# Optimization experiments

Measured on AMD Instinct MI355X. Metric: run time of the kernel, lower is better.

Reference implementation:

```python
import jax, jax.numpy as jnp
import numpy as np

N_NODES = 100000
NEG_SLOPE = 0.2


def _gat_conv(x, edge_index, W, att_src, att_dst, bias):
    """Single-head PyG-style GATConv with self-loops.
    x: [N, F_in], edge_index: [2, E] (row 0 = src j, row 1 = dst i).
    """
    N = x.shape[0]
    h = x @ W  # [N, F_out]
    # add self-loops
    loop = jnp.arange(N, dtype=edge_index.dtype)
    src = jnp.concatenate([edge_index[0], loop])
    dst = jnp.concatenate([edge_index[1], loop])
    # per-node attention terms, gathered per edge
    a_s = h @ att_src  # [N]
    a_d = h @ att_dst  # [N]
    e = jax.nn.leaky_relu(a_s[src] + a_d[dst], NEG_SLOPE)  # [E+N]
    # segment softmax over incoming edges of each destination
    m = jax.ops.segment_max(e, dst, num_segments=N)  # [N]
    m = jnp.where(jnp.isfinite(m), m, 0.0)
    p = jnp.exp(e - m[dst])
    denom = jax.ops.segment_sum(p, dst, num_segments=N)  # [N], >0 due to self-loops
    alpha = p / denom[dst]  # [E+N]
    # scatter-aggregate weighted source features
    out = jax.ops.segment_sum(h[src] * alpha[:, None], dst, num_segments=N)
    return out + bias


def setup_inputs() -> dict:
    key = jax.random.key(0)
    ks = jax.random.split(key, 12)
    F_in, H, C = 128, 64, 40
    x = jax.random.normal(ks[0], (N_NODES, F_in), dtype=jnp.float32)
    edge_index = jax.random.randint(ks[1], (2, 1600000), 0, N_NODES, dtype=jnp.int64)
    s1 = 1.0 / np.sqrt(F_in)
    s2 = 1.0 / np.sqrt(H)
    return {
        "x": x,
        "edge_index": edge_index,
        "W1": jax.random.uniform(ks[2], (F_in, H), jnp.float32, -s1, s1),
        "att_src1": jax.random.uniform(ks[3], (H,), jnp.float32, -s2, s2),
        "att_dst1": jax.random.uniform(ks[4], (H,), jnp.float32, -s2, s2),
        "b1": jnp.zeros((H,), jnp.float32),
        "W2": jax.random.uniform(ks[5], (H, C), jnp.float32, -s2, s2),
        "att_src2": jax.random.uniform(ks[6], (C,), jnp.float32, -1.0 / np.sqrt(C), 1.0 / np.sqrt(C)),
        "att_dst2": jax.random.uniform(ks[7], (C,), jnp.float32, -1.0 / np.sqrt(C), 1.0 / np.sqrt(C)),
        "b2": jnp.zeros((C,), jnp.float32),
    }


def reference(x, edge_index, W1, att_src1, att_dst1, b1, W2, att_src2, att_dst2, b2):
    h = _gat_conv(x, edge_index, W1, att_src1, att_dst1, b1)
    h = jax.nn.relu(h)
    # dropout is identity in eval mode
    out = _gat_conv(h, edge_index, W2, att_src2, att_dst2, b2)
    return out
```

## Files before the change

kernel.cpp:

```cpp
#include <hip/hip_runtime.h>
#include <math.h>


#define NEG_SLOPE 0.2f
#define BIN_SHIFT 10
#define BIN_NODES 1024
#define MAXBINS   128
#define CAPB      17408
#define K1_CHUNK  4096
#define MAXDEG    128
#define AGG_STRIDE 132

typedef _Float16 h4_t __attribute__((ext_vector_type(4)));
typedef _Float16 h8_t __attribute__((ext_vector_type(8)));
typedef float    f16x_t __attribute__((ext_vector_type(16)));

__device__ __forceinline__ float lrelu(float v) {
    return v > 0.f ? v : NEG_SLOPE * v;
}

__global__ __launch_bounds__(256) void prep_kernel(
    const float* __restrict__ W1, const float* __restrict__ W2,
    _Float16* __restrict__ w1t, _Float16* __restrict__ w2t)
{
    const int tid = threadIdx.x;
    for (int i = tid; i < 8192; i += 256) {
        int n = i >> 7, k = i & 127;
        w1t[i] = (_Float16)W1[k * 64 + n];
    }
    for (int i = tid; i < 4096; i += 256) {
        int n = i >> 6, k = i & 63;
        w2t[i] = (n < 40) ? (_Float16)W2[k * 40 + n] : (_Float16)0.f;
    }
}

__global__ __launch_bounds__(256) void bin_kernel(
    const int* __restrict__ src, const int* __restrict__ dst, int E, int nbins,
    int* __restrict__ bin_cursor, int* __restrict__ binned)
{
    __shared__ int hist[MAXBINS];
    __shared__ int base[MAXBINS];
    __shared__ int lcur[MAXBINS];
    const int tid = threadIdx.x;
    const int e0 = blockIdx.x * K1_CHUNK;

    if (tid < nbins) hist[tid] = 0;
    __syncthreads();

    for (int k = tid; k < K1_CHUNK; k += 256) {
        int e = e0 + k;
        if (e < E) atomicAdd(&hist[dst[e] >> BIN_SHIFT], 1);
    }
    __syncthreads();

    if (tid < nbins) {
        int c = hist[tid];
        base[tid] = (c > 0) ? atomicAdd(&bin_cursor[tid], c) : 0;
        lcur[tid] = 0;
    }
    __syncthreads();

    for (int k = tid; k < K1_CHUNK; k += 256) {
        int e = e0 + k;
        if (e < E) {
            int d = dst[e];
            int s = src[e];
            int b = d >> BIN_SHIFT;
            int o = atomicAdd(&lcur[b], 1);
            int pos = base[b] + o;
            if (pos < CAPB)
                binned[b * CAPB + pos] = (s << BIN_SHIFT) | (d & (BIN_NODES - 1));
        }
    }
}

__global__ __launch_bounds__(128) void scan_kernel(
    const int* __restrict__ bin_cursor, int* __restrict__ bin_base, int nbins)
{
    __shared__ int a[MAXBINS];
    const int tid = threadIdx.x;
    int v = (tid < nbins) ? min(bin_cursor[tid], CAPB) : 0;
    a[tid] = v;
    __syncthreads();
#pragma unroll
    for (int ofs = 1; ofs < 128; ofs <<= 1) {
        int t = (tid >= ofs) ? a[tid - ofs] : 0;
        __syncthreads();
        a[tid] += t;
        __syncthreads();
    }
    if (tid < nbins) bin_base[tid] = a[tid] - v;
}

__global__ __launch_bounds__(1024) void fine_kernel(
    const int* __restrict__ bin_cursor, const int* __restrict__ bin_base,
    const int* __restrict__ binned,
    int* __restrict__ csr, int* __restrict__ rowptr, int N, int nbins)
{
    __shared__ int a[BIN_NODES];
    __shared__ int cur[BIN_NODES];
    const int b = blockIdx.x;
    const int tid = threadIdx.x;

    const int cnt = min(bin_cursor[b], CAPB);
    const int binbase = bin_base[b];
    const int nn = min(BIN_NODES, N - b * BIN_NODES);
    const int* __restrict__ brec = binned + (long)b * CAPB;

    a[tid] = 0;
    __syncthreads();

    for (int k = tid; k < cnt; k += 1024) {
        atomicAdd(&a[brec[k] & (BIN_NODES - 1)], 1);
    }
    __syncthreads();

    int v = a[tid];
#pragma unroll
    for (int ofs = 1; ofs < BIN_NODES; ofs <<= 1) {
        int t = (tid >= ofs) ? a[tid - ofs] : 0;
        __syncthreads();
        a[tid] += t;
        __syncthreads();
    }
    const int excl = a[tid] - v;

    if (tid < nn) rowptr[b * BIN_NODES + tid] = binbase + excl;
    cur[tid] = binbase + excl;
    if (b == nbins - 1 && tid == 0) rowptr[N] = binbase + cnt;
    __syncthreads();

    for (int k = tid; k < cnt; k += 1024) {
        int rec = brec[k];
        int pos = atomicAdd(&cur[rec & (BIN_NODES - 1)], 1);
        csr[pos] = rec >> BIN_SHIFT;
    }
}

#define XS1 136
__global__ __launch_bounds__(256) void gemm1_kernel(
    const float* __restrict__ x, const _Float16* __restrict__ w1t,
    const float* __restrict__ att_s, const float* __restrict__ att_d,
    _Float16* __restrict__ h, float* __restrict__ as_, float* __restrict__ ad_,
    int N)
{
    __shared__ __align__(16) _Float16 Xs[64 * XS1];
    __shared__ __align__(16) _Float16 Wt[64 * XS1];
    __shared__ float psrow[64], pdrow[64];
    const int tid = threadIdx.x;
    const int lane = tid & 63;
    const int w = tid >> 6;
    const int rh = w >> 1, ch = w & 1;
    const long rowbase = (long)blockIdx.x * 64;

    {
        const int4* src = (const int4*)w1t;
#pragma unroll
        for (int i = 0; i < 4; ++i) {
            int f = tid + i * 256;
            int n = f >> 4, c = f & 15;
            *(int4*)&Wt[n * XS1 + c * 8] = src[f];
        }
    }
    {
        const float4* X4 = (const float4*)x;
        const long gmax = (long)N * 32;
#pragma unroll
        for (int i = 0; i < 8; ++i) {
            int f = tid + i * 256;
            int row = f >> 5, c4 = f & 31;
            long gi = (rowbase + row) * 32 + c4;
            float4 v = (gi < gmax) ? X4[gi] : make_float4(0.f, 0.f, 0.f, 0.f);
            h4_t hv;
            hv.x = (_Float16)v.x; hv.y = (_Float16)v.y;
            hv.z = (_Float16)v.z; hv.w = (_Float16)v.w;
            *(h4_t*)&Xs[row * XS1 + c4 * 4] = hv;
        }
    }
    if (tid < 64) { psrow[tid] = 0.f; pdrow[tid] = 0.f; }
    __syncthreads();

    const int m = lane & 31, khalf = lane >> 5;
    const _Float16* ax = &Xs[(rh * 32 + m) * XS1 + khalf * 8];
    const _Float16* bx = &Wt[(ch * 32 + m) * XS1 + khalf * 8];

    f16x_t acc = {};
#pragma unroll
    for (int kc = 0; kc < 8; ++kc) {
        h8_t a = *(const h8_t*)(ax + kc * 16);
        h8_t b = *(const h8_t*)(bx + kc * 16);
        acc = __builtin_amdgcn_mfma_f32_32x32x16_f16(a, b, acc, 0, 0, 0);
    }

    const int col = ch * 32 + m;
    const float asc = att_s[col], adc = att_d[col];
#pragma unroll
    for (int r = 0; r < 16; ++r) {
        int rowl = (r & 3) + 8 * (r >> 2) + 4 * khalf;
        long grow = rowbase + rh * 32 + rowl;
        float v = acc[r];
        if (grow < N) h[grow * 64 + col] = (_Float16)v;
        float ps = v * asc, pd = v * adc;
#pragma unroll
        for (int off = 1; off < 32; off <<= 1) {
            ps += __shfl_xor(ps, off);
            pd += __shfl_xor(pd, off);
        }
        if (m == 0) {
            atomicAdd(&psrow[rh * 32 + rowl], ps);
            atomicAdd(&pdrow[rh * 32 + rowl], pd);
        }
    }
    __syncthreads();
    if (tid < 64) {
        long grow = rowbase + tid;
        if (grow < N) { as_[grow] = psrow[tid]; ad_[grow] = pdrow[tid]; }
    }
}

#define XS2 72
__global__ __launch_bounds__(256) void gemm2_kernel(
    const _Float16* __restrict__ hin, const _Float16* __restrict__ w2t,
    const float* __restrict__ att_s, const float* __restrict__ att_d,
    _Float16* __restrict__ h2, float* __restrict__ as_, float* __restrict__ ad_,
    int N)
{
    __shared__ __align__(16) _Float16 Xs[64 * XS2];
    __shared__ __align__(16) _Float16 Wt[64 * XS2];
    __shared__ float psrow[64], pdrow[64];
    const int tid = threadIdx.x;
    const int lane = tid & 63;
    const int w = tid >> 6;
    const int rh = w >> 1, ch = w & 1;
    const long rowbase = (long)blockIdx.x * 64;

    {
        const int4* src = (const int4*)w2t;
#pragma unroll
        for (int i = 0; i < 2; ++i) {
            int f = tid + i * 256;
            int n = f >> 3, c = f & 7;
            *(int4*)&Wt[n * XS2 + c * 8] = src[f];
        }
    }
    {
        const h8_t* X8 = (const h8_t*)hin;
        const long gmax = (long)N * 8;
#pragma unroll
        for (int i = 0; i < 2; ++i) {
            int f = tid + i * 256;
            int row = f >> 3, c = f & 7;
            long gi = (rowbase + row) * 8 + c;
            h8_t v = {};
            if (gi < gmax) v = X8[gi];
#pragma unroll
            for (int j = 0; j < 8; ++j) v[j] = (v[j] > (_Float16)0.f) ? v[j] : (_Float16)0.f;
            *(h8_t*)&Xs[row * XS2 + c * 8] = v;
        }
    }
    if (tid < 64) { psrow[tid] = 0.f; pdrow[tid] = 0.f; }
    __syncthreads();

    const int m = lane & 31, khalf = lane >> 5;
    const _Float16* ax = &Xs[(rh * 32 + m) * XS2 + khalf * 8];
    const _Float16* bx = &Wt[(ch * 32 + m) * XS2 + khalf * 8];

    f16x_t acc = {};
#pragma unroll
    for (int kc = 0; kc < 4; ++kc) {
        h8_t a = *(const h8_t*)(ax + kc * 16);
        h8_t b = *(const h8_t*)(bx + kc * 16);
        acc = __builtin_amdgcn_mfma_f32_32x32x16_f16(a, b, acc, 0, 0, 0);
    }

    const int col = ch * 32 + m;
    const bool cval = (col < 40);
    const float asc = cval ? att_s[col] : 0.f;
    const float adc = cval ? att_d[col] : 0.f;
#pragma unroll
    for (int r = 0; r < 16; ++r) {
        int rowl = (r & 3) + 8 * (r >> 2) + 4 * khalf;
        long grow = rowbase + rh * 32 + rowl;
        float v = acc[r];
        if (cval && grow < N) h2[grow * 40 + col] = (_Float16)v;
        float ps = v * asc, pd = v * adc;
#pragma unroll
        for (int off = 1; off < 32; off <<= 1) {
            ps += __shfl_xor(ps, off);
            pd += __shfl_xor(pd, off);
        }
        if (m == 0) {
            atomicAdd(&psrow[rh * 32 + rowl], ps);
            atomicAdd(&pdrow[rh * 32 + rowl], pd);
        }
    }
    __syncthreads();
    if (tid < 64) {
        long grow = rowbase + tid;
        if (grow < N) { as_[grow] = psrow[tid]; ad_[grow] = pdrow[tid]; }
    }
}

template<int F, typename OT>
__global__ __launch_bounds__(256) void aggregate_kernel(
    const _Float16* __restrict__ h, const float* __restrict__ as_,
    const float* __restrict__ ad_, const int* __restrict__ rowptr,
    const int* __restrict__ csr, const float* __restrict__ bias,
    OT* __restrict__ out, int N)
{
    __shared__ int   Ss[16 * AGG_STRIDE];
    __shared__ float Ps[16 * AGG_STRIDE];
    const int tid = threadIdx.x;
    const int dl  = tid >> 4;
    const int sub = tid & 15;
    const int i = blockIdx.x * 16 + dl;
    const bool alive = (i < N);

    int r0 = 0, deg = 0;
    if (alive) {
        r0 = rowptr[i];
        deg = rowptr[i + 1] - r0;
        if (deg > MAXDEG) deg = MAXDEG;
    }
    const float adi    = alive ? ad_[i] : 0.f;
    const float e_self = alive ? lrelu(as_[i] + adi) : 0.f;

    int*   __restrict__ sp = &Ss[dl * AGG_STRIDE];
    float* __restrict__ pp = &Ps[dl * AGG_STRIDE];

    float psum = 0.f;
    for (int c = sub; c < deg; c += 16) {
        int s = csr[r0 + c];
        float p = __expf(lrelu(as_[s] + adi));
        sp[c] = s;
        pp[c] = p;
        psum += p;
    }
#pragma unroll
    for (int off = 1; off < 16; off <<= 1) psum += __shfl_xor(psum, off);
    const float p_self = __expf(e_self);
    const float inv = 1.f / (psum + p_self);

    const bool act = (sub * 4 < F);
    const int  col = act ? sub * 4 : 0;
    float4 acc = make_float4(0.f, 0.f, 0.f, 0.f);

    int k = 0;
    for (; k + 4 <= deg; k += 4) {
        int   sA = sp[k],     sB = sp[k + 1], sC = sp[k + 2], sD = sp[k + 3];
        float pA = pp[k],     pB = pp[k + 1], pC = pp[k + 2], pD = pp[k + 3];
        if (act) {
            h4_t hA = *(const h4_t*)&h[(long)sA * F + col];
            h4_t hB = *(const h4_t*)&h[(long)sB * F + col];
            h4_t hC = *(const h4_t*)&h[(long)sC * F + col];
            h4_t hD = *(const h4_t*)&h[(long)sD * F + col];
            acc.x += (float)hA.x * pA + (float)hB.x * pB + (float)hC.x * pC + (float)hD.x * pD;
            acc.y += (float)hA.y * pA + (float)hB.y * pB + (float)hC.y * pC + (float)hD.y * pD;
            acc.z += (float)hA.z * pA + (float)hB.z * pB + (float)hC.z * pC + (float)hD.z * pD;
            acc.w += (float)hA.w * pA + (float)hB.w * pB + (float)hC.w * pC + (float)hD.w * pD;
        }
    }
    for (; k < deg; ++k) {
        int   s = sp[k];
        float p = pp[k];
        if (act) {
            h4_t hv = *(const h4_t*)&h[(long)s * F + col];
            acc.x += (float)hv.x * p; acc.y += (float)hv.y * p;
            acc.z += (float)hv.z * p; acc.w += (float)hv.w * p;
        }
    }

    if (alive && act) {
        h4_t hv = *(const h4_t*)&h[(long)i * F + col];
        float4 bv = *(const float4*)&bias[col];
        float ox = (acc.x + (float)hv.x * p_self) * inv + bv.x;
        float oy = (acc.y + (float)hv.y * p_self) * inv + bv.y;
        float oz = (acc.z + (float)hv.z * p_self) * inv + bv.z;
        float ow = (acc.w + (float)hv.w * p_self) * inv + bv.w;
        if constexpr (sizeof(OT) == 4) {
            float4 o = make_float4(ox, oy, oz, ow);
            *(float4*)&out[(long)i * F + col] = o;
        } else {
            h4_t o;
            o.x = (_Float16)ox; o.y = (_Float16)oy;
            o.z = (_Float16)oz; o.w = (_Float16)ow;
            *(h4_t*)&out[(long)i * F + col] = o;
        }
    }
}

extern "C" void kernel_launch(void* const* d_in, const int* in_sizes, int n_in,
                              void* d_out, int out_size, void* d_ws, size_t ws_size,
                              hipStream_t stream) {
    const float* x    = (const float*)d_in[0];
    const int*   ei   = (const int*)d_in[1];
    const float* W1   = (const float*)d_in[2];
    const float* at_s1= (const float*)d_in[3];
    const float* at_d1= (const float*)d_in[4];
    const float* b1   = (const float*)d_in[5];
    const float* W2   = (const float*)d_in[6];
    const float* at_s2= (const float*)d_in[7];
    const float* at_d2= (const float*)d_in[8];
    const float* b2   = (const float*)d_in[9];
    float* out = (float*)d_out;

    const int N = in_sizes[0] / 128;
    const int E = in_sizes[1] / 2;
    const int nbins = (N + BIN_NODES - 1) >> BIN_SHIFT;

    char* p = (char*)d_ws;
    auto carve = [&](size_t bytes) -> void* {
        void* r = (void*)p;
        p += (bytes + 255) & ~(size_t)255;
        return r;
    };
    int*       bin_cursor = (int*)      carve((size_t)MAXBINS * 4);
    int*       bin_base   = (int*)      carve((size_t)MAXBINS * 4);
    int*       binned     = (int*)      carve((size_t)nbins * CAPB * 4);
    int*       csr        = (int*)      carve((size_t)E * 4);
    int*       rowptr     = (int*)      carve((size_t)(N + 1) * 4);
    _Float16*  w1t        = (_Float16*) carve((size_t)8192 * 2);
    _Float16*  w2t        = (_Float16*) carve((size_t)4096 * 2);
    _Float16*  h1         = (_Float16*) carve((size_t)N * 64 * 2);
    _Float16*  agg1h      = (_Float16*) carve((size_t)N * 64 * 2);
    _Float16*  h2         = (_Float16*) carve((size_t)N * 40 * 2);
    float*     asn        = (float*)    carve((size_t)N * 4);
    float*     adn        = (float*)    carve((size_t)N * 4);

    hipMemsetAsync(bin_cursor, 0, (size_t)MAXBINS * 4, stream);

    prep_kernel<<<1, 256, 0, stream>>>(W1, W2, w1t, w2t);
    bin_kernel<<<(E + K1_CHUNK - 1) / K1_CHUNK, 256, 0, stream>>>(
        ei, ei + E, E, nbins, bin_cursor, binned);
    scan_kernel<<<1, 128, 0, stream>>>(bin_cursor, bin_base, nbins);
    fine_kernel<<<nbins, 1024, 0, stream>>>(bin_cursor, bin_base, binned, csr, rowptr, N, nbins);

    gemm1_kernel<<<(N + 63) / 64, 256, 0, stream>>>(x, w1t, at_s1, at_d1, h1, asn, adn, N);
    aggregate_kernel<64, _Float16><<<(N + 15) / 16, 256, 0, stream>>>(
        h1, asn, adn, rowptr, csr, b1, agg1h, N);

    gemm2_kernel<<<(N + 63) / 64, 256, 0, stream>>>(agg1h, w2t, at_s2, at_d2, h2, asn, adn, N);
    aggregate_kernel<40, float><<<(N + 15) / 16, 256, 0, stream>>>(
        h2, asn, adn, rowptr, csr, b2, out, N);
}
```

Baseline: 271.6 us.

## Fuse gemm1 with edge binning and fold attention vectors into weights

Attention projections are precomputed as W·att vectors. Layer 1 computes a_s/a_d directly from x with a small dot product. Layer 2 appends them as two extra MFMA output columns in the padded weight tile, which removes the per-row shuffle reductions and LDS atomics. The gemm1 and edge-binning kernels are merged into a single launch with a block-range split so both run concurrently, and the binning path now preloads its edges into registers. The cost is a larger shared-memory footprint for the merged kernel, plus extra fp16 rounding of the folded attention vectors in layer 2 and of x in layer 1.

Result: faster. 241.4 us (-11.1%).

```diff
diff --git a/kernel.cpp b/kernel.cpp
--- a/kernel.cpp
+++ b/kernel.cpp
@@ -10,6 +10,7 @@
 #define K1_CHUNK  4096
 #define MAXDEG    128
 #define AGG_STRIDE 132
+#define XS1 136
 
 typedef _Float16 h4_t __attribute__((ext_vector_type(4)));
 typedef _Float16 h8_t __attribute__((ext_vector_type(8)));
@@ -21,55 +22,175 @@
 
 __global__ __launch_bounds__(256) void prep_kernel(
     const float* __restrict__ W1, const float* __restrict__ W2,
-    _Float16* __restrict__ w1t, _Float16* __restrict__ w2t)
-{
-    const int tid = threadIdx.x;
-    for (int i = tid; i < 8192; i += 256) {
-        int n = i >> 7, k = i & 127;
-        w1t[i] = (_Float16)W1[k * 64 + n];
-    }
-    for (int i = tid; i < 4096; i += 256) {
-        int n = i >> 6, k = i & 63;
-        w2t[i] = (n < 40) ? (_Float16)W2[k * 40 + n] : (_Float16)0.f;
-    }
-}
-
-__global__ __launch_bounds__(256) void bin_kernel(
+    const float* __restrict__ as1, const float* __restrict__ ad1,
+    const float* __restrict__ as2, const float* __restrict__ ad2,
+    _Float16* __restrict__ w1t, _Float16* __restrict__ w2t,
+    float* __restrict__ u1, float* __restrict__ v1)
+{
+    const int tid = threadIdx.x;
+    if (blockIdx.x == 0) {
+        for (int i = tid; i < 8192; i += 256) {
+            int n = i >> 7, k = i & 127;
+            w1t[i] = (_Float16)W1[k * 64 + n];
+        }
+        if (tid < 128) {
+            float su = 0.f, sv = 0.f;
+            for (int n = 0; n < 64; ++n) {
+                float w = W1[tid * 64 + n];
+                su += w * as1[n];
+                sv += w * ad1[n];
+            }
+            u1[tid] = su; v1[tid] = sv;
+        }
+    } else {
+        __shared__ float u2l[64], v2l[64];
+        if (tid < 64) {
+            float su = 0.f, sv = 0.f;
+            for (int n = 0; n < 40; ++n) {
+                float w = W2[tid * 40 + n];
+                su += w * as2[n];
+                sv += w * ad2[n];
+            }
+            u2l[tid] = su; v2l[tid] = sv;
+        }
+        __syncthreads();
+        for (int i = tid; i < 4096; i += 256) {
+            int n = i >> 6, k = i & 63;
+            _Float16 o = (_Float16)0.f;
+            if (n < 40)       o = (_Float16)W2[k * 40 + n];
+            else if (n == 40) o = (_Float16)u2l[k];
+            else if (n == 41) o = (_Float16)v2l[k];
+            w2t[i] = o;
+        }
+    }
+}
+
+__global__ __launch_bounds__(256) void gemm1_bin_kernel(
+    const float* __restrict__ x, const _Float16* __restrict__ w1t,
+    const float* __restrict__ u1, const float* __restrict__ v1,
+    _Float16* __restrict__ h, float* __restrict__ as_, float* __restrict__ ad_,
+    int N, int gb,
     const int* __restrict__ src, const int* __restrict__ dst, int E, int nbins,
     int* __restrict__ bin_cursor, int* __restrict__ binned)
 {
-    __shared__ int hist[MAXBINS];
-    __shared__ int base[MAXBINS];
-    __shared__ int lcur[MAXBINS];
-    const int tid = threadIdx.x;
-    const int e0 = blockIdx.x * K1_CHUNK;
-
-    if (tid < nbins) hist[tid] = 0;
-    __syncthreads();
-
-    for (int k = tid; k < K1_CHUNK; k += 256) {
-        int e = e0 + k;
-        if (e < E) atomicAdd(&hist[dst[e] >> BIN_SHIFT], 1);
-    }
-    __syncthreads();
-
-    if (tid < nbins) {
-        int c = hist[tid];
-        base[tid] = (c > 0) ? atomicAdd(&bin_cursor[tid], c) : 0;
-        lcur[tid] = 0;
-    }
-    __syncthreads();
-
-    for (int k = tid; k < K1_CHUNK; k += 256) {
-        int e = e0 + k;
-        if (e < E) {
-            int d = dst[e];
-            int s = src[e];
-            int b = d >> BIN_SHIFT;
-            int o = atomicAdd(&lcur[b], 1);
-            int pos = base[b] + o;
-            if (pos < CAPB)
-                binned[b * CAPB + pos] = (s << BIN_SHIFT) | (d & (BIN_NODES - 1));
+    __shared__ __align__(16) char smem[35840];
+    const int tid = threadIdx.x;
+
+    if (blockIdx.x < gb) {
+        _Float16* Xs = (_Float16*)smem;
+        _Float16* Wt = (_Float16*)(smem + 17408);
+        float*    Us = (float*)(smem + 34816);
+        float*    Vs = (float*)(smem + 35328);
+        const int lane = tid & 63;
+        const int w = tid >> 6;
+        const int rh = w >> 1, ch = w & 1;
+        const long rowbase = (long)blockIdx.x * 64;
+
+        {
+            const int4* s4 = (const int4*)w1t;
+#pragma unroll
+            for (int i = 0; i < 4; ++i) {
+                int f = tid + i * 256;
+                int n = f >> 4, c = f & 15;
+                *(int4*)&Wt[n * XS1 + c * 8] = s4[f];
+            }
+        }
+        {
+            const float4* X4 = (const float4*)x;
+            const long gmax = (long)N * 32;
+#pragma unroll
+            for (int i = 0; i < 8; ++i) {
+                int f = tid + i * 256;
+                int row = f >> 5, c4 = f & 31;
+                long gi = (rowbase + row) * 32 + c4;
+                float4 v = (gi < gmax) ? X4[gi] : make_float4(0.f, 0.f, 0.f, 0.f);
+                h4_t hv;
+                hv.x = (_Float16)v.x; hv.y = (_Float16)v.y;
+                hv.z = (_Float16)v.z; hv.w = (_Float16)v.w;
+                *(h4_t*)&Xs[row * XS1 + c4 * 4] = hv;
+            }
+        }
+        if (tid < 128) Us[tid] = u1[tid];
+        else { int t = tid - 128; Vs[t] = v1[t]; }
+        __syncthreads();
+
+        {
+            const int arow = tid >> 2, apart = tid & 3;
+            const _Float16* xr = &Xs[arow * XS1 + apart * 32];
+            float ps = 0.f, pd = 0.f;
+#pragma unroll
+            for (int k = 0; k < 32; k += 4) {
+                h4_t xv = *(const h4_t*)(xr + k);
+                float4 uu = *(const float4*)&Us[apart * 32 + k];
+                float4 vv = *(const float4*)&Vs[apart * 32 + k];
+                float x0 = (float)xv.x, x1 = (float)xv.y, x2 = (float)xv.z, x3 = (float)xv.w;
+                ps += x0 * uu.x + x1 * uu.y + x2 * uu.z + x3 * uu.w;
+                pd += x0 * vv.x + x1 * vv.y + x2 * vv.z + x3 * vv.w;
+            }
+            ps += __shfl_xor(ps, 1); ps += __shfl_xor(ps, 2);
+            pd += __shfl_xor(pd, 1); pd += __shfl_xor(pd, 2);
+            if (apart == 0 && rowbase + arow < N) {
+                as_[rowbase + arow] = ps;
+                ad_[rowbase + arow] = pd;
+            }
+        }
+
+        const int m = lane & 31, khalf = lane >> 5;
+        const _Float16* ax = &Xs[(rh * 32 + m) * XS1 + khalf * 8];
+        const _Float16* bx = &Wt[(ch * 32 + m) * XS1 + khalf * 8];
+
+        f16x_t acc = {};
+#pragma unroll
+        for (int kc = 0; kc < 8; ++kc) {
+            h8_t a = *(const h8_t*)(ax + kc * 16);
+            h8_t b = *(const h8_t*)(bx + kc * 16);
+            acc = __builtin_amdgcn_mfma_f32_32x32x16_f16(a, b, acc, 0, 0, 0);
+        }
+
+        const int col = ch * 32 + m;
+#pragma unroll
+        for (int r = 0; r < 16; ++r) {
+            int rowl = (r & 3) + 8 * (r >> 2) + 4 * khalf;
+            long grow = rowbase + rh * 32 + rowl;
+            if (grow < N) h[grow * 64 + col] = (_Float16)acc[r];
+        }
+    } else {
+        int* hist = (int*)smem;
+        int* base = (int*)(smem + 512);
+        int* lcur = (int*)(smem + 1024);
+        const int e0 = (blockIdx.x - gb) * K1_CHUNK;
+
+        int sreg[16], dreg[16];
+#pragma unroll
+        for (int k = 0; k < 16; ++k) {
+            int e = e0 + tid + k * 256;
+            bool ok = e < E;
+            dreg[k] = ok ? dst[e] : -1;
+            sreg[k] = ok ? src[e] : 0;
+        }
+
+        if (tid < nbins) hist[tid] = 0;
+        __syncthreads();
+#pragma unroll
+        for (int k = 0; k < 16; ++k)
+            if (dreg[k] >= 0) atomicAdd(&hist[dreg[k] >> BIN_SHIFT], 1);
+        __syncthreads();
+        if (tid < nbins) {
+            int c = hist[tid];
+            base[tid] = (c > 0) ? atomicAdd(&bin_cursor[tid], c) : 0;
+            lcur[tid] = 0;
+        }
+        __syncthreads();
+#pragma unroll
+        for (int k = 0; k < 16; ++k) {
+            if (dreg[k] >= 0) {
+                int b = dreg[k] >> BIN_SHIFT;
+                int o = atomicAdd(&lcur[b], 1);
+                int pos = base[b] + o;
+                if (pos < CAPB)
+                    binned[b * CAPB + pos] =
+                        (sreg[k] << BIN_SHIFT) | (dreg[k] & (BIN_NODES - 1));
+            }
         }
     }
 }
@@ -137,16 +258,14 @@
     }
 }
 
-#define XS1 136
-__global__ __launch_bounds__(256) void gemm1_kernel(
-    const float* __restrict__ x, const _Float16* __restrict__ w1t,
-    const float* __restrict__ att_s, const float* __restrict__ att_d,
-    _Float16* __restrict__ h, float* __restrict__ as_, float* __restrict__ ad_,
+#define XS2 72
+__global__ __launch_bounds__(256) void gemm2_kernel(
+    const _Float16* __restrict__ hin, const _Float16* __restrict__ w2t,
+    _Float16* __restrict__ h2, float* __restrict__ as_, float* __restrict__ ad_,
     int N)
 {
-    __shared__ __align__(16) _Float16 Xs[64 * XS1];
-    __shared__ __align__(16) _Float16 Wt[64 * XS1];
-    __shared__ float psrow[64], pdrow[64];
+    __shared__ __align__(16) _Float16 Xs[64 * XS2];
+    __shared__ __align__(16) _Float16 Wt[64 * XS2];
     const int tid = threadIdx.x;
     const int lane = tid & 63;
     const int w = tid >> 6;
@@ -154,93 +273,12 @@
     const long rowbase = (long)blockIdx.x * 64;
 
     {
-        const int4* src = (const int4*)w1t;
-#pragma unroll
-        for (int i = 0; i < 4; ++i) {
-            int f = tid + i * 256;
-            int n = f >> 4, c = f & 15;
-            *(int4*)&Wt[n * XS1 + c * 8] = src[f];
-        }
-    }
-    {
-        const float4* X4 = (const float4*)x;
-        const long gmax = (long)N * 32;
-#pragma unroll
-        for (int i = 0; i < 8; ++i) {
-            int f = tid + i * 256;
-            int row = f >> 5, c4 = f & 31;
-            long gi = (rowbase + row) * 32 + c4;
-            float4 v = (gi < gmax) ? X4[gi] : make_float4(0.f, 0.f, 0.f, 0.f);
-            h4_t hv;
-            hv.x = (_Float16)v.x; hv.y = (_Float16)v.y;
-            hv.z = (_Float16)v.z; hv.w = (_Float16)v.w;
-            *(h4_t*)&Xs[row * XS1 + c4 * 4] = hv;
-        }
-    }
-    if (tid < 64) { psrow[tid] = 0.f; pdrow[tid] = 0.f; }
-    __syncthreads();
-
-    const int m = lane & 31, khalf = lane >> 5;
-    const _Float16* ax = &Xs[(rh * 32 + m) * XS1 + khalf * 8];
-    const _Float16* bx = &Wt[(ch * 32 + m) * XS1 + khalf * 8];
-
-    f16x_t acc = {};
-#pragma unroll
-    for (int kc = 0; kc < 8; ++kc) {
-        h8_t a = *(const h8_t*)(ax + kc * 16);
-        h8_t b = *(const h8_t*)(bx + kc * 16);
-        acc = __builtin_amdgcn_mfma_f32_32x32x16_f16(a, b, acc, 0, 0, 0);
-    }
-
-    const int col = ch * 32 + m;
-    const float asc = att_s[col], adc = att_d[col];
-#pragma unroll
-    for (int r = 0; r < 16; ++r) {
-        int rowl = (r & 3) + 8 * (r >> 2) + 4 * khalf;
-        long grow = rowbase + rh * 32 + rowl;
-        float v = acc[r];
-        if (grow < N) h[grow * 64 + col] = (_Float16)v;
-        float ps = v * asc, pd = v * adc;
-#pragma unroll
-        for (int off = 1; off < 32; off <<= 1) {
-            ps += __shfl_xor(ps, off);
-            pd += __shfl_xor(pd, off);
-        }
-        if (m == 0) {
-            atomicAdd(&psrow[rh * 32 + rowl], ps);
-            atomicAdd(&pdrow[rh * 32 + rowl], pd);
-        }
-    }
-    __syncthreads();
-    if (tid < 64) {
-        long grow = rowbase + tid;
-        if (grow < N) { as_[grow] = psrow[tid]; ad_[grow] = pdrow[tid]; }
-    }
-}
-
-#define XS2 72
-__global__ __launch_bounds__(256) void gemm2_kernel(
-    const _Float16* __restrict__ hin, const _Float16* __restrict__ w2t,
-    const float* __restrict__ att_s, const float* __restrict__ att_d,
-    _Float16* __restrict__ h2, float* __restrict__ as_, float* __restrict__ ad_,
-    int N)
-{
-    __shared__ __align__(16) _Float16 Xs[64 * XS2];
-    __shared__ __align__(16) _Float16 Wt[64 * XS2];
-    __shared__ float psrow[64], pdrow[64];
-    const int tid = threadIdx.x;
-    const int lane = tid & 63;
-    const int w = tid >> 6;
-    const int rh = w >> 1, ch = w & 1;
-    const long rowbase = (long)blockIdx.x * 64;
-
-    {
-        const int4* src = (const int4*)w2t;
+        const int4* s4 = (const int4*)w2t;
 #pragma unroll
         for (int i = 0; i < 2; ++i) {
             int f = tid + i * 256;
             int n = f >> 3, c = f & 7;
-            *(int4*)&Wt[n * XS2 + c * 8] = src[f];
+            *(int4*)&Wt[n * XS2 + c * 8] = s4[f];
         }
     }
     {
@@ -258,7 +296,6 @@
             *(h8_t*)&Xs[row * XS2 + c * 8] = v;
         }
     }
-    if (tid < 64) { psrow[tid] = 0.f; pdrow[tid] = 0.f; }
     __syncthreads();
 
     const int m = lane & 31, khalf = lane >> 5;
@@ -274,30 +311,16 @@
     }
 
     const int col = ch * 32 + m;
-    const bool cval = (col < 40);
-    const float asc = cval ? att_s[col] : 0.f;
-    const float adc = cval ? att_d[col] : 0.f;
 #pragma unroll
     for (int r = 0; r < 16; ++r) {
         int rowl = (r & 3) + 8 * (r >> 2) + 4 * khalf;
         long grow = rowbase + rh * 32 + rowl;
         float v = acc[r];
-        if (cval && grow < N) h2[grow * 40 + col] = (_Float16)v;
-        float ps = v * asc, pd = v * adc;
-#pragma unroll
-        for (int off = 1; off < 32; off <<= 1) {
-            ps += __shfl_xor(ps, off);
-            pd += __shfl_xor(pd, off);
-        }
-        if (m == 0) {
-            atomicAdd(&psrow[rh * 32 + rowl], ps);
-            atomicAdd(&pdrow[rh * 32 + rowl], pd);
-        }
-    }
-    __syncthreads();
-    if (tid < 64) {
-        long grow = rowbase + tid;
-        if (grow < N) { as_[grow] = psrow[tid]; ad_[grow] = pdrow[tid]; }
+        if (grow < N) {
+            if (col < 40)       h2[grow * 40 + col] = (_Float16)v;
+            else if (col == 40) as_[grow] = v;
+            else if (col == 41) ad_[grow] = v;
+        }
     }
 }
 
@@ -421,6 +444,8 @@
     int*       rowptr     = (int*)      carve((size_t)(N + 1) * 4);
     _Float16*  w1t        = (_Float16*) carve((size_t)8192 * 2);
     _Float16*  w2t        = (_Float16*) carve((size_t)4096 * 2);
+    float*     u1         = (float*)    carve((size_t)128 * 4);
+    float*     v1         = (float*)    carve((size_t)128 * 4);
     _Float16*  h1         = (_Float16*) carve((size_t)N * 64 * 2);
     _Float16*  agg1h      = (_Float16*) carve((size_t)N * 64 * 2);
     _Float16*  h2         = (_Float16*) carve((size_t)N * 40 * 2);
@@ -429,17 +454,23 @@
 
     hipMemsetAsync(bin_cursor, 0, (size_t)MAXBINS * 4, stream);
 
-    prep_kernel<<<1, 256, 0, stream>>>(W1, W2, w1t, w2t);
-    bin_kernel<<<(E + K1_CHUNK - 1) / K1_CHUNK, 256, 0, stream>>>(
+    prep_kernel<<<2, 256, 0, stream>>>(W1, W2, at_s1, at_d1, at_s2, at_d2,
+                                       w1t, w2t, u1, v1);
+
+    const int gb = (N + 63) / 64;
+    const int bb = (E + K1_CHUNK - 1) / K1_CHUNK;
+    gemm1_bin_kernel<<<gb + bb, 256, 0, stream>>>(
+        x, w1t, u1, v1, h1, asn, adn, N, gb,
         ei, ei + E, E, nbins, bin_cursor, binned);
+
     scan_kernel<<<1, 128, 0, stream>>>(bin_cursor, bin_base, nbins);
     fine_kernel<<<nbins, 1024, 0, stream>>>(bin_cursor, bin_base, binned, csr, rowptr, N, nbins);
 
-    gemm1_kernel<<<(N + 63) / 64, 256, 0, stream>>>(x, w1t, at_s1, at_d1, h1, asn, adn, N);
     aggregate_kernel<64, _Float16><<<(N + 15) / 16, 256, 0, stream>>>(
         h1, asn, adn, rowptr, csr, b1, agg1h, N);
 
-    gemm2_kernel<<<(N + 63) / 64, 256, 0, stream>>>(agg1h, w2t, at_s2, at_d2, h2, asn, adn, N);
+    gemm2_kernel<<<(N + 63) / 64, 256, 0, stream>>>(agg1h, w2t, h2, asn, adn, N);
+
     aggregate_kernel<40, float><<<(N + 15) / 16, 256, 0, stream>>>(
         h2, asn, adn, rowptr, csr, b2, out, N);
 }
```
